# Performance work log

Hardware: AMD Instinct MI355X
Metric: run time of the kernel (lower is better)

The kernel has to match this reference:

```python
import jax, jax.numpy as jnp
import numpy as np

T = 1024
H = 256
W = 256
D1 = 512
D2 = 1024


def setup_inputs() -> dict:
    key = jax.random.key(0)
    ks = jax.random.split(key, 8)
    B = 16
    x_true = jax.random.normal(ks[0], (B, H, W), dtype=jnp.float32)
    k_points = 0.25 * jax.random.normal(ks[1], (T, 2), dtype=jnp.float32)
    # torch Linear default init ~ U(-1/sqrt(fan_in), 1/sqrt(fan_in)); scale suffices
    def lin(k, fi, fo):
        s = 1.0 / np.sqrt(fi)
        return jax.random.uniform(k, (fi, fo), jnp.float32, -s, s)
    W1 = lin(ks[2], 2 * T, D1)
    b1 = jnp.zeros((D1,), jnp.float32)
    W2 = lin(ks[3], D1, D2)
    b2 = jnp.zeros((D2,), jnp.float32)
    W3 = lin(ks[4], D2, H * W)
    b3 = jnp.zeros((H * W,), jnp.float32)
    return {"x_true": x_true, "k_points": k_points, "W1": W1, "b1": b1,
            "W2": W2, "b2": b2, "W3": W3, "b3": b3}


def _fourier_sample(x, k_points):
    # phase[t,h,w] = exp(-2pi i (kx[t]*xx[w] + ky[t]*yy[h])) = px[t,w]*py[t,h]
    xx = jnp.linspace(-0.5, 0.5, W)  # (W,)
    yy = jnp.linspace(-0.5, 0.5, H)  # (H,)
    two_pi = 2.0 * jnp.pi
    px = jnp.exp(-1j * two_pi * k_points[:, 0:1] * xx[None, :])  # (T, W) complex
    py = jnp.exp(-1j * two_pi * k_points[:, 1:2] * yy[None, :])  # (T, H) complex
    # samples[b,t] = sum_{h,w} x[b,h,w] * px[t,w] * py[t,h]
    a = jnp.einsum('bhw,tw->bth', x.astype(jnp.complex64), px)  # (B, T, H)
    return jnp.einsum('bth,th->bt', a, py)  # (B, T) complex


def reference(x_true, k_points, W1, b1, W2, b2, W3, b3):
    y = _fourier_sample(x_true, k_points)  # (B, T) complex
    feat = jnp.concatenate([y.real, y.imag], axis=-1)  # (B, 2T)
    h1 = jax.nn.relu(feat @ W1 + b1)
    h2 = jax.nn.relu(h1 @ W2 + b2)
    out = h2 @ W3 + b3
    x_hat = out.reshape(x_true.shape[0], H, W)
    return (x_hat, y, k_points)
```

## Files before the change

kernel.cpp:

```cpp
#include <hip/hip_runtime.h>
#include <hip/hip_bf16.h>
#include <math.h>

#define WS_PB     0u
#define WS_PYRE   262144u
#define WS_PYIM   524288u
#define WS_XB     786432u
#define WS_FEAT   1310720u
#define WS_H1ACC  1343488u
#define WS_H1F    1351680u
#define WS_H2ACC  1359872u
#define WS_H2T    1376256u
#define WS_PT     1392640u

#define OUT_Y  1048576

typedef __attribute__((ext_vector_type(8))) short short8;
typedef __attribute__((ext_vector_type(4))) float f32x4;

__device__ inline unsigned short f2bf(float f) {
  __hip_bfloat16 h = __float2bfloat16(f);
  return *reinterpret_cast<unsigned short*>(&h);
}

__global__ void k0_cvt(const float* __restrict__ x, unsigned short* __restrict__ xb) {
  int i = (blockIdx.x * 256 + threadIdx.x) * 4;
  float4 v = *(const float4*)(x + i);
  ushort4 o;
  o.x = f2bf(v.x); o.y = f2bf(v.y); o.z = f2bf(v.z); o.w = f2bf(v.w);
  *(ushort4*)(xb + i) = o;
}

__global__ void k1_trig(const float* __restrict__ kp, unsigned short* __restrict__ Pb,
                        float* __restrict__ pyre, float* __restrict__ pyim) {
  int bid = blockIdx.x, tid = threadIdx.x;
  const float TWO_PI = 6.28318530717958647692f;
  if (bid < 1024) {
    int t = bid, w = tid;
    float kx = kp[2 * t];
    float xx = -0.5f + (float)w * (1.0f / 255.0f);
    float s, c;
    sincosf(TWO_PI * kx * xx, &s, &c);
    Pb[t * 256 + w]          = f2bf(c);
    Pb[(1024 + t) * 256 + w] = f2bf(-s);
  } else {
    int t = bid - 1024, h = tid;
    float ky = kp[2 * t + 1];
    float yy = -0.5f + (float)h * (1.0f / 255.0f);
    float s, c;
    sincosf(TWO_PI * ky * yy, &s, &c);
    pyre[t * 256 + h] = c;
    pyim[t * 256 + h] = -s;
  }
}

#define TPAD 40

__launch_bounds__(256)
__global__ void k23_fused(const unsigned short* __restrict__ Pb,
                          const unsigned short* __restrict__ xb,
                          const float* __restrict__ pyre, const float* __restrict__ pyim,
                          float* __restrict__ feat, float* __restrict__ out_y,
                          float* __restrict__ h1_acc, int ymode) {
  __shared__ unsigned short Alds[64 * TPAD];
  __shared__ unsigned short Xlds[256 * TPAD];
  __shared__ float red[32][4][4];
  int tid = threadIdx.x;
  int b  = blockIdx.y;
  int t0 = blockIdx.x * 32;
  int w = tid >> 6, l = tid & 63;
  int g = l >> 4, c = l & 15;
  const unsigned short* xbase = xb + (size_t)b * 65536;

  f32x4 acc[4][4] = {};

  for (int ks = 0; ks < 8; ++ks) {
    int k0 = ks * 32;
    __syncthreads();
    {
      int row = tid >> 2, seg = tid & 3;
      int trow = (row < 32) ? (t0 + row) : (1024 + t0 + row - 32);
      *(uint4*)(&Alds[row * TPAD + seg * 8]) =
          *(const uint4*)(Pb + (size_t)trow * 256 + k0 + seg * 8);
    }
    {
      const unsigned short* src = xbase + (size_t)tid * 256 + k0;
      unsigned short* dst = &Xlds[tid * TPAD];
      *(uint4*)(dst)      = *(const uint4*)(src);
      *(uint4*)(dst + 8)  = *(const uint4*)(src + 8);
      *(uint4*)(dst + 16) = *(const uint4*)(src + 16);
      *(uint4*)(dst + 24) = *(const uint4*)(src + 24);
    }
    __syncthreads();
    short8 afr[4], bfr[4];
    #pragma unroll
    for (int mf = 0; mf < 4; ++mf)
      afr[mf] = *reinterpret_cast<const short8*>(&Alds[(mf * 16 + c) * TPAD + g * 8]);
    #pragma unroll
    for (int hf = 0; hf < 4; ++hf)
      bfr[hf] = *reinterpret_cast<const short8*>(&Xlds[(w * 64 + hf * 16 + c) * TPAD + g * 8]);
    #pragma unroll
    for (int mf = 0; mf < 4; ++mf)
      #pragma unroll
      for (int hf = 0; hf < 4; ++hf)
        acc[mf][hf] = __builtin_amdgcn_mfma_f32_16x16x32_bf16(afr[mf], bfr[hf], acc[mf][hf], 0, 0, 0);
  }

  float srr[2][4] = {{0}}, sii[2][4] = {{0}}, sri[2][4] = {{0}}, sir[2][4] = {{0}};
  #pragma unroll
  for (int mh = 0; mh < 2; ++mh)
    #pragma unroll
    for (int r = 0; r < 4; ++r) {
      int t = t0 + mh * 16 + g * 4 + r;
      #pragma unroll
      for (int hf = 0; hf < 4; ++hf) {
        int h = w * 64 + hf * 16 + c;
        float cr = pyre[t * 256 + h], ci = pyim[t * 256 + h];
        float vre = acc[mh][hf][r], vim = acc[mh + 2][hf][r];
        srr[mh][r] += vre * cr; sri[mh][r] += vre * ci;
        sir[mh][r] += vim * cr; sii[mh][r] += vim * ci;
      }
    }
  #pragma unroll
  for (int mh = 0; mh < 2; ++mh)
    #pragma unroll
    for (int r = 0; r < 4; ++r) {
      float a0 = srr[mh][r], a1 = sii[mh][r], a2 = sri[mh][r], a3 = sir[mh][r];
      #pragma unroll
      for (int off = 1; off < 16; off <<= 1) {
        a0 += __shfl_xor(a0, off, 64);
        a1 += __shfl_xor(a1, off, 64);
        a2 += __shfl_xor(a2, off, 64);
        a3 += __shfl_xor(a3, off, 64);
      }
      if (c == 0) {
        int tloc = mh * 16 + g * 4 + r;
        red[tloc][w][0] = a0; red[tloc][w][1] = a1;
        red[tloc][w][2] = a2; red[tloc][w][3] = a3;
      }
    }
  __syncthreads();
  if (tid < 32) {
    int t = t0 + tid;
    float yre = 0.f, yim = 0.f;
    #pragma unroll
    for (int ww = 0; ww < 4; ++ww) {
      yre += red[tid][ww][0] - red[tid][ww][1];
      yim += red[tid][ww][2] + red[tid][ww][3];
    }
    feat[b * 2048 + t]        = yre;
    feat[b * 2048 + 1024 + t] = yim;
    if (ymode == 0) {
      out_y[b * 1024 + t] = yre;
    } else {
      out_y[(b * 1024 + t) * 2]     = yre;
      out_y[(b * 1024 + t) * 2 + 1] = yim;
    }
  }
  if (blockIdx.y == 0) h1_acc[blockIdx.x * 256 + tid] = 0.f;
}

__global__ void k4_w1(const float* __restrict__ feat, const float* __restrict__ W1,
                      float* __restrict__ h1_acc) {
  int nt = blockIdx.x & 1, ks = blockIdx.x >> 1;
  int n = nt * 256 + threadIdx.x;
  int k0 = ks * 64;
  float acc[16];
  #pragma unroll
  for (int b = 0; b < 16; ++b) acc[b] = 0.f;
  for (int k = k0; k < k0 + 64; ++k) {
    float w = W1[k * 512 + n];
    #pragma unroll
    for (int b = 0; b < 16; ++b) acc[b] += feat[b * 2048 + k] * w;
  }
  #pragma unroll
  for (int b = 0; b < 16; ++b) atomicAdd(&h1_acc[b * 512 + n], acc[b]);
}

__global__ void k4b_fin(const float* __restrict__ h1_acc, const float* __restrict__ b1,
                        float* __restrict__ h1f, float* __restrict__ h2_acc) {
  int i = blockIdx.x * 256 + threadIdx.x;
  if (i < 8192) {
    int k = i & 511;
    h1f[i] = fmaxf(h1_acc[i] + b1[k], 0.f);
  }
  if (i < 16384) h2_acc[i] = 0.f;
}

__global__ void k5_w2(const float* __restrict__ h1f, const float* __restrict__ W2,
                      float* __restrict__ h2_acc) {
  int nt = blockIdx.x & 3, ks = blockIdx.x >> 2;
  int n = nt * 256 + threadIdx.x;
  int k0 = ks * 32;
  float acc[16];
  #pragma unroll
  for (int b = 0; b < 16; ++b) acc[b] = 0.f;
  for (int k = k0; k < k0 + 32; ++k) {
    float w = W2[k * 1024 + n];
    #pragma unroll
    for (int b = 0; b < 16; ++b) acc[b] += h1f[b * 512 + k] * w;
  }
  #pragma unroll
  for (int b = 0; b < 16; ++b) atomicAdd(&h2_acc[b * 1024 + n], acc[b]);
}

__global__ void k5b_fin(const float* __restrict__ h2_acc, const float* __restrict__ b2,
                        const float* __restrict__ kp, float* __restrict__ h2t,
                        float* __restrict__ out_kp) {
  int i = blockIdx.x * 256 + threadIdx.x;
  if (i < 16384) {
    int k = i >> 4, b = i & 15;
    h2t[i] = fmaxf(h2_acc[b * 1024 + k] + b2[k], 0.f);
  } else {
    int j = i - 16384;
    out_kp[j] = kp[j];
  }
}

__launch_bounds__(256, 2)
__global__ void k6_w3(const float* __restrict__ h2t, const float* __restrict__ W3,
                      float* __restrict__ pt) {
  __shared__ float hs[256][16];
  int tid = threadIdx.x;
  int kc = blockIdx.y;
  int k0 = kc * 256;
  int n = blockIdx.x * 512 + tid * 2;
  {
    const float4* src = (const float4*)(h2t + (size_t)(k0 + tid) * 16);
    float4* dst = (float4*)hs[tid];
    dst[0] = src[0]; dst[1] = src[1]; dst[2] = src[2]; dst[3] = src[3];
  }
  __syncthreads();
  float accx[16] = {}, accy[16] = {};
  const float* w3p = W3 + (size_t)k0 * 65536 + n;
  #pragma unroll 8
  for (int k = 0; k < 256; ++k) {
    float2 w = *(const float2*)(w3p + (size_t)k * 65536);
    const float* hr = hs[k];
    #pragma unroll
    for (int b = 0; b < 16; ++b) {
      accx[b] += hr[b] * w.x;
      accy[b] += hr[b] * w.y;
    }
  }
  float* pb = pt + (size_t)kc * 16 * 65536 + n;
  #pragma unroll
  for (int b = 0; b < 16; ++b)
    *(float2*)(pb + (size_t)b * 65536) = make_float2(accx[b], accy[b]);
}

__global__ void k6b_red(const float* __restrict__ pt, const float* __restrict__ b3,
                        float* __restrict__ out) {
  int i = (blockIdx.x * 256 + threadIdx.x) * 4;
  int n = i & 65535;
  float4 s = *(const float4*)(b3 + n);
  #pragma unroll
  for (int kc = 0; kc < 4; ++kc) {
    float4 p = *(const float4*)(pt + (size_t)kc * 1048576 + i);
    s.x += p.x; s.y += p.y; s.z += p.z; s.w += p.w;
  }
  *(float4*)(out + i) = s;
}

extern "C" void kernel_launch(void* const* d_in, const int* in_sizes, int n_in,
                              void* d_out, int out_size, void* d_ws, size_t ws_size,
                              hipStream_t stream) {
  const float* x  = (const float*)d_in[0];
  const float* kp = (const float*)d_in[1];
  const float* W1 = (const float*)d_in[2];
  const float* b1 = (const float*)d_in[3];
  const float* W2 = (const float*)d_in[4];
  const float* b2 = (const float*)d_in[5];
  const float* W3 = (const float*)d_in[6];
  const float* b3 = (const float*)d_in[7];
  float* out = (float*)d_out;
  float* ws  = (float*)d_ws;

  unsigned short* Pb = (unsigned short*)(ws + WS_PB);
  float* pyre   = ws + WS_PYRE;
  float* pyim   = ws + WS_PYIM;
  unsigned short* xb = (unsigned short*)(ws + WS_XB);
  float* feat   = ws + WS_FEAT;
  float* h1_acc = ws + WS_H1ACC;
  float* h1f    = ws + WS_H1F;
  float* h2_acc = ws + WS_H2ACC;
  float* h2t    = ws + WS_H2T;
  float* pt     = ws + WS_PT;

  int ymode = (out_size == 1048576 + 16384 + 2048) ? 0 : 1;
  float* out_y  = out + OUT_Y;
  float* out_kp = out + (out_size - 2048);

  k0_cvt<<<dim3(1024), dim3(256), 0, stream>>>(x, xb);
  k1_trig<<<dim3(2048), dim3(256), 0, stream>>>(kp, Pb, pyre, pyim);
  k23_fused<<<dim3(32, 16), dim3(256), 0, stream>>>(Pb, xb, pyre, pyim, feat, out_y, h1_acc, ymode);
  k4_w1<<<dim3(64), dim3(256), 0, stream>>>(feat, W1, h1_acc);
  k4b_fin<<<dim3(96), dim3(256), 0, stream>>>(h1_acc, b1, h1f, h2_acc);
  k5_w2<<<dim3(64), dim3(256), 0, stream>>>(h1f, W2, h2_acc);
  k5b_fin<<<dim3(72), dim3(256), 0, stream>>>(h2_acc, b2, kp, h2t, out_kp);
  k6_w3<<<dim3(128, 4), dim3(256), 0, stream>>>(h2t, W3, pt);
  k6b_red<<<dim3(1024), dim3(256), 0, stream>>>(pt, b3, out);
}
```

Before: 439.6 us.

## Fuse x bf16 conversion into Fourier GEMM and double k-split for W3

Removes the standalone fp32-to-bf16 conversion kernel for x and converts it while staging into LDS inside the fused Fourier GEMM. Each block now rereads fp32 x, twice the bytes, and the x buffer leaves the workspace. The W3 GEMM's k-split goes from 4 to 8 chunks with a higher occupancy hint, doubling blocks to better use the CUs. This raises partial-sum traffic, since the reduction kernel now reads 8 partial buffers instead of 4.

```diff
diff --git a/kernel.cpp b/kernel.cpp
--- a/kernel.cpp
+++ b/kernel.cpp
@@ -5,13 +5,12 @@
 #define WS_PB     0u
 #define WS_PYRE   262144u
 #define WS_PYIM   524288u
-#define WS_XB     786432u
-#define WS_FEAT   1310720u
-#define WS_H1ACC  1343488u
-#define WS_H1F    1351680u
-#define WS_H2ACC  1359872u
-#define WS_H2T    1376256u
-#define WS_PT     1392640u
+#define WS_FEAT   786432u
+#define WS_H1ACC  819200u
+#define WS_H1F    827392u
+#define WS_H2ACC  835584u
+#define WS_H2T    851968u
+#define WS_PT     868352u
 
 #define OUT_Y  1048576
 
@@ -21,14 +20,6 @@
 __device__ inline unsigned short f2bf(float f) {
   __hip_bfloat16 h = __float2bfloat16(f);
   return *reinterpret_cast<unsigned short*>(&h);
-}
-
-__global__ void k0_cvt(const float* __restrict__ x, unsigned short* __restrict__ xb) {
-  int i = (blockIdx.x * 256 + threadIdx.x) * 4;
-  float4 v = *(const float4*)(x + i);
-  ushort4 o;
-  o.x = f2bf(v.x); o.y = f2bf(v.y); o.z = f2bf(v.z); o.w = f2bf(v.w);
-  *(ushort4*)(xb + i) = o;
 }
 
 __global__ void k1_trig(const float* __restrict__ kp, unsigned short* __restrict__ Pb,
@@ -58,7 +49,7 @@
 
 __launch_bounds__(256)
 __global__ void k23_fused(const unsigned short* __restrict__ Pb,
-                          const unsigned short* __restrict__ xb,
+                          const float* __restrict__ x,
                           const float* __restrict__ pyre, const float* __restrict__ pyim,
                           float* __restrict__ feat, float* __restrict__ out_y,
                           float* __restrict__ h1_acc, int ymode) {
@@ -70,7 +61,7 @@
   int t0 = blockIdx.x * 32;
   int w = tid >> 6, l = tid & 63;
   int g = l >> 4, c = l & 15;
-  const unsigned short* xbase = xb + (size_t)b * 65536;
+  const float* xbase = x + (size_t)b * 65536;
 
   f32x4 acc[4][4] = {};
 
@@ -84,12 +75,15 @@
           *(const uint4*)(Pb + (size_t)trow * 256 + k0 + seg * 8);
     }
     {
-      const unsigned short* src = xbase + (size_t)tid * 256 + k0;
+      const float* src = xbase + (size_t)tid * 256 + k0;
       unsigned short* dst = &Xlds[tid * TPAD];
-      *(uint4*)(dst)      = *(const uint4*)(src);
-      *(uint4*)(dst + 8)  = *(const uint4*)(src + 8);
-      *(uint4*)(dst + 16) = *(const uint4*)(src + 16);
-      *(uint4*)(dst + 24) = *(const uint4*)(src + 24);
+      #pragma unroll
+      for (int j = 0; j < 8; ++j) {
+        float4 v = *(const float4*)(src + j * 4);
+        ushort4 o;
+        o.x = f2bf(v.x); o.y = f2bf(v.y); o.z = f2bf(v.z); o.w = f2bf(v.w);
+        *(ushort4*)(dst + j * 4) = o;
+      }
     }
     __syncthreads();
     short8 afr[4], bfr[4];
@@ -217,24 +211,25 @@
   }
 }
 
-__launch_bounds__(256, 2)
+__launch_bounds__(256, 4)
 __global__ void k6_w3(const float* __restrict__ h2t, const float* __restrict__ W3,
                       float* __restrict__ pt) {
-  __shared__ float hs[256][16];
+  __shared__ float hs[128][16];
   int tid = threadIdx.x;
   int kc = blockIdx.y;
-  int k0 = kc * 256;
+  int k0 = kc * 128;
   int n = blockIdx.x * 512 + tid * 2;
   {
-    const float4* src = (const float4*)(h2t + (size_t)(k0 + tid) * 16);
-    float4* dst = (float4*)hs[tid];
-    dst[0] = src[0]; dst[1] = src[1]; dst[2] = src[2]; dst[3] = src[3];
+    int r = tid >> 1, half = tid & 1;
+    const float4* src = (const float4*)(h2t + (size_t)(k0 + r) * 16 + half * 8);
+    float4* dst = (float4*)(&hs[r][half * 8]);
+    dst[0] = src[0]; dst[1] = src[1];
   }
   __syncthreads();
   float accx[16] = {}, accy[16] = {};
   const float* w3p = W3 + (size_t)k0 * 65536 + n;
   #pragma unroll 8
-  for (int k = 0; k < 256; ++k) {
+  for (int k = 0; k < 128; ++k) {
     float2 w = *(const float2*)(w3p + (size_t)k * 65536);
     const float* hr = hs[k];
     #pragma unroll
@@ -243,7 +238,7 @@
       accy[b] += hr[b] * w.y;
     }
   }
-  float* pb = pt + (size_t)kc * 16 * 65536 + n;
+  float* pb = pt + (size_t)kc * 1048576 + n;
   #pragma unroll
   for (int b = 0; b < 16; ++b)
     *(float2*)(pb + (size_t)b * 65536) = make_float2(accx[b], accy[b]);
@@ -255,7 +250,7 @@
   int n = i & 65535;
   float4 s = *(const float4*)(b3 + n);
   #pragma unroll
-  for (int kc = 0; kc < 4; ++kc) {
+  for (int kc = 0; kc < 8; ++kc) {
     float4 p = *(const float4*)(pt + (size_t)kc * 1048576 + i);
     s.x += p.x; s.y += p.y; s.z += p.z; s.w += p.w;
   }
@@ -279,7 +274,6 @@
   unsigned short* Pb = (unsigned short*)(ws + WS_PB);
   float* pyre   = ws + WS_PYRE;
   float* pyim   = ws + WS_PYIM;
-  unsigned short* xb = (unsigned short*)(ws + WS_XB);
   float* feat   = ws + WS_FEAT;
   float* h1_acc = ws + WS_H1ACC;
   float* h1f    = ws + WS_H1F;
@@ -291,13 +285,12 @@
   float* out_y  = out + OUT_Y;
   float* out_kp = out + (out_size - 2048);
 
-  k0_cvt<<<dim3(1024), dim3(256), 0, stream>>>(x, xb);
   k1_trig<<<dim3(2048), dim3(256), 0, stream>>>(kp, Pb, pyre, pyim);
-  k23_fused<<<dim3(32, 16), dim3(256), 0, stream>>>(Pb, xb, pyre, pyim, feat, out_y, h1_acc, ymode);
+  k23_fused<<<dim3(32, 16), dim3(256), 0, stream>>>(Pb, x, pyre, pyim, feat, out_y, h1_acc, ymode);
   k4_w1<<<dim3(64), dim3(256), 0, stream>>>(feat, W1, h1_acc);
   k4b_fin<<<dim3(96), dim3(256), 0, stream>>>(h1_acc, b1, h1f, h2_acc);
   k5_w2<<<dim3(64), dim3(256), 0, stream>>>(h1f, W2, h2_acc);
   k5b_fin<<<dim3(72), dim3(256), 0, stream>>>(h2_acc, b2, kp, h2t, out_kp);
-  k6_w3<<<dim3(128, 4), dim3(256), 0, stream>>>(h2t, W3, pt);
+  k6_w3<<<dim3(128, 8), dim3(256), 0, stream>>>(h2t, W3, pt);
   k6b_red<<<dim3(1024), dim3(256), 0, stream>>>(pt, b3, out);
 }
```

Result: no change. 442.1 us (+0.6%).
